# Performance work log

Measured on AMD Instinct MI355X. Metric: run time of the kernel, lower is better.

Reference implementation:

```python
import jax, jax.numpy as jnp
import numpy as np

N_CAT = 100000
N_USERS = 50000
D = 64
N_REL = 16  # edge_type in [1, 15]; weight has n_relations-1 = 15 rows
E = 1500000
NNZ = 1500000


def setup_inputs() -> dict:
    key = jax.random.key(0)
    k = jax.random.split(key, 8)
    category_emb = jax.random.normal(k[0], (N_CAT, D), dtype=jnp.float32)
    user_emb = jax.random.normal(k[1], (N_USERS, D), dtype=jnp.float32)
    edge_index = jax.random.randint(k[2], (2, E), 0, N_CAT, dtype=jnp.int32)
    edge_type = jax.random.randint(k[3], (E,), 1, N_REL, dtype=jnp.int32)  # [1, 15]
    iu = jax.random.randint(k[4], (NNZ,), 0, N_USERS, dtype=jnp.int32)
    ic = jax.random.randint(k[5], (NNZ,), 0, N_CAT, dtype=jnp.int32)
    interact_idx = jnp.stack([iu, ic], axis=0)
    interact_val = jax.random.uniform(k[6], (NNZ,), dtype=jnp.float32)
    weight = jax.random.normal(k[7], (N_REL - 1, D), dtype=jnp.float32) * (6.0 / (N_REL - 1 + D)) ** 0.5
    return {"category_emb": category_emb, "user_emb": user_emb,
            "edge_index": edge_index, "edge_type": edge_type,
            "interact_idx": interact_idx, "interact_val": interact_val,
            "weight": weight}


def reference(category_emb, user_emb, edge_index, edge_type, interact_idx, interact_val, weight):
    n_cat = category_emb.shape[0]
    n_users = user_emb.shape[0]
    head, tail = edge_index[0], edge_index[1]

    # per-edge relation embedding gather
    rel = weight[edge_type - 1]                       # [E, d]
    neigh = category_emb[tail] * rel                  # [E, d]

    # norm-based attention score per edge: (||h*r|| * ||t*r||)^2
    hn = jnp.linalg.norm(category_emb[head] * rel, axis=1)   # [E]
    tn = jnp.linalg.norm(neigh, axis=1)                      # [E]
    att = (hn * tn) ** 2                                     # [E]

    # scatter-softmax over head segments (score is constant across feature dim)
    seg_max = jax.ops.segment_max(att, head, num_segments=n_cat)
    e = jnp.exp(att - seg_max[head])
    seg_sum = jax.ops.segment_sum(e, head, num_segments=n_cat)
    w = e / seg_sum[head]                                    # [E]

    # scatter-sum aggregation of weighted neighbor messages
    category_agg = jax.ops.segment_sum(w[:, None] * neigh, head, num_segments=n_cat)  # [n_cat, d]

    # sparse-dense matmul: interact_mat @ category_emb (COO gather + segment_sum)
    iu, ic = interact_idx[0], interact_idx[1]
    user_agg = jax.ops.segment_sum(interact_val[:, None] * category_emb[ic], iu,
                                   num_segments=n_users)     # [n_users, d]

    # relation-score gating of user aggregation
    score = jax.nn.softmax(user_emb @ weight.T, axis=-1)     # [n_users, n_rel-1]
    user_agg = user_agg + (score @ weight) * user_agg
    return category_agg, user_agg
```

## Files before the change

kernel.cpp:

```cpp
#include <hip/hip_runtime.h>

#define N_CAT   100000
#define N_USERS 50000
#define DIM     64
#define N_RELM1 15
#define E_EDGES 1500000
#define NNZ_E   1500000

#define HPB   125
#define NB_H  800
#define UPB   80
#define NB_U  625
#define NB_T  (NB_H + NB_U)
#define CAP8  3072

#define NS_TILES 1563
#define GT_TILES 782

#define BIN_BLKS 256
#define BIN_CH   5860

#define NTL(p) __builtin_nontemporal_load(p)

__device__ __forceinline__ float sb2f(unsigned int v, int sh) {
    return (float)(int)(signed char)((v >> sh) & 0xFFu);
}

template <bool USE8>
__global__ void __launch_bounds__(256)
prep_kernel(const float* __restrict__ cat, const float* __restrict__ uemb,
            const float* __restrict__ weight,
            const int* __restrict__ head, const int* __restrict__ iu,
            float* __restrict__ normsq, unsigned int* __restrict__ cat8,
            float* __restrict__ scl,
            float* __restrict__ gfac, int* __restrict__ gcnt,
            int* __restrict__ cnts_cat, int* __restrict__ cnts_u0,
            int* __restrict__ cnts_u1) {
    __shared__ float smem[8320];
    int t = threadIdx.x;
    int lane = t & 63, wid = t >> 6;
    if (blockIdx.x < NS_TILES) {
        float* c2    = smem;
        float* w2t   = smem + 4160;
        float* nsqT  = smem + 5184;
        float* rinv  = smem + 6208;
        float* rmaxp = smem + 6272;
        int nbase = blockIdx.x * 64;
        int nclamp = min(64, N_CAT - nbase);
        for (int i = t; i < 1024; i += 256) {
            int d = i >> 4, r = i & 15;
            float w = (r < N_RELM1) ? weight[r * 64 + d] : 0.f;
            w2t[i] = w * w;
        }
        for (int i = t; i < 4096; i += 256) {
            int row = i >> 6, d = i & 63;
            float v = (row < nclamp) ? cat[(size_t)(nbase + row) * 64 + d] : 0.f;
            c2[row * 65 + d] = v;
        }
        __syncthreads();
        if (USE8) {
            {
                int row = t >> 2, part = t & 3;
                float m = 0.f;
#pragma unroll
                for (int d = part * 16; d < part * 16 + 16; ++d)
                    m = fmaxf(m, fabsf(c2[row * 65 + d]));
                rmaxp[t] = m;
            }
            __syncthreads();
            if (t < 64) {
                float m = fmaxf(fmaxf(rmaxp[4 * t], rmaxp[4 * t + 1]),
                                fmaxf(rmaxp[4 * t + 2], rmaxp[4 * t + 3]));
                rinv[t] = (m > 0.f) ? 127.f / m : 0.f;
                if (t < nclamp) scl[nbase + t] = (m > 0.f) ? m / 127.f : 0.f;
            }
            __syncthreads();
            for (int i = t; i < 1024; i += 256) {
                int row = i >> 4, q4 = i & 15;
                if (row < nclamp) {
                    float inv = rinv[row];
                    int d0 = q4 * 4;
                    unsigned int p = 0;
#pragma unroll
                    for (int k = 0; k < 4; ++k) {
                        int q = (int)rintf(c2[row * 65 + d0 + k] * inv);
                        p |= ((unsigned int)(q & 0xFF)) << (8 * k);
                    }
                    cat8[(size_t)(nbase + row) * 16 + q4] = p;
                }
            }
        }
        float a0 = 0, a1 = 0, a2 = 0, a3 = 0;
        int r0 = wid * 4;
#pragma unroll 8
        for (int d = 0; d < 64; ++d) {
            float c = c2[lane * 65 + d];
            float cc = c * c;
            float4 w4 = *(float4*)&w2t[d * 16 + r0];
            a0 += cc * w4.x; a1 += cc * w4.y; a2 += cc * w4.z; a3 += cc * w4.w;
        }
        nsqT[(r0 + 0) * 64 + lane] = a0;
        nsqT[(r0 + 1) * 64 + lane] = a1;
        nsqT[(r0 + 2) * 64 + lane] = a2;
        nsqT[(r0 + 3) * 64 + lane] = a3;
        __syncthreads();
        for (int i = t; i < nclamp * 15; i += 256) {
            int n = i / 15, r = i - n * 15;
            normsq[(size_t)(nbase + n) * 15 + r] = nsqT[r * 64 + n];
        }
    } else if (blockIdx.x < NS_TILES + GT_TILES) {
        float* ut  = smem;
        float* wt  = smem + 4160;
        float* wrT = smem + 5184;
        float* st  = smem + 6208;
        float* pt  = smem + 7232;
        int ub_ = (blockIdx.x - NS_TILES) * 64;
        int uclamp = min(64, N_USERS - ub_);
        for (int i = t; i < 1024; i += 256) {
            int d = i >> 4, r = i & 15;
            float w = (r < N_RELM1) ? weight[r * 64 + d] : 0.f;
            wt[i] = w;
            wrT[r * 64 + d] = w;
        }
        for (int i = t; i < 4096; i += 256) {
            int row = i >> 6, d = i & 63;
            ut[row * 65 + d] = (row < uclamp) ? uemb[(size_t)(ub_ + row) * 64 + d] : 0.f;
        }
        __syncthreads();
        float a0 = 0, a1 = 0, a2 = 0, a3 = 0;
        int r0 = wid * 4;
#pragma unroll 8
        for (int d = 0; d < 64; ++d) {
            float c = ut[lane * 65 + d];
            float4 w4 = *(float4*)&wt[d * 16 + r0];
            a0 += c * w4.x; a1 += c * w4.y; a2 += c * w4.z; a3 += c * w4.w;
        }
        st[lane * 16 + r0 + 0] = a0;
        st[lane * 16 + r0 + 1] = a1;
        st[lane * 16 + r0 + 2] = a2;
        st[lane * 16 + r0 + 3] = a3;
        __syncthreads();
        if (wid == 0) {
            float mx = -1e30f;
            float pv[N_RELM1];
#pragma unroll
            for (int r = 0; r < N_RELM1; ++r) mx = fmaxf(mx, st[lane * 16 + r]);
            float Z = 0.f;
#pragma unroll
            for (int r = 0; r < N_RELM1; ++r) { pv[r] = __expf(st[lane * 16 + r] - mx); Z += pv[r]; }
            float inv = 1.f / Z;
#pragma unroll
            for (int r = 0; r < N_RELM1; ++r) pt[lane * 16 + r] = pv[r] * inv;
        }
        __syncthreads();
        for (int i = t; i < uclamp * 64; i += 256) {
            int u = i >> 6, d = i & 63;
            float g = 0.f;
#pragma unroll
            for (int r = 0; r < N_RELM1; ++r) g += pt[u * 16 + r] * wrT[r * 64 + d];
            gfac[(size_t)(ub_ + u) * 64 + d] = g;
        }
    } else {
        int* ccnt = (int*)smem;
        int* cu0  = ccnt + NB_H;
        int* cu1  = cu0 + 640;
        for (int i = t; i < NB_H + 1280; i += 256) ccnt[i] = 0;
        __syncthreads();
        int hb = blockIdx.x - NS_TILES - GT_TILES;
        int c0 = hb * BIN_CH;
        int c1 = min(c0 + BIN_CH, E_EDGES);
        int hmid = c0 + BIN_CH / 2;
        for (int e = c0 + t; e < c1; e += 256) {
            atomicAdd(&ccnt[NTL(&head[e]) / HPB], 1);
            int ub = NTL(&iu[e]) / UPB;
            atomicAdd((e < hmid) ? &cu0[ub] : &cu1[ub], 1);
        }
        __syncthreads();
        for (int i = t; i < NB_H; i += 256) {
            int v = ccnt[i];
            cnts_cat[hb * NB_H + i] = v;
            if (v) atomicAdd(&gcnt[i], v);
        }
        for (int j = t; j < NB_U; j += 256) {
            int v0 = cu0[j], v1 = cu1[j];
            cnts_u0[hb * 640 + j] = v0;
            cnts_u1[hb * 640 + j] = v1;
            if (v0 + v1) atomicAdd(&gcnt[NB_H + j], v0 + v1);
        }
    }
}

__global__ void __launch_bounds__(1024)
bscan_kernel(const int* __restrict__ gcnt,
             int* __restrict__ hbase, int* __restrict__ ubase,
             int* __restrict__ cur) {
    __shared__ int wtot[16];
    int t = threadIdx.x, lane = t & 63, wv = t >> 6;
    int i0 = 2 * t, i1 = 2 * t + 1;
    int c0 = (i0 < NB_T) ? gcnt[i0] : 0;
    int c1 = (i1 < NB_T) ? gcnt[i1] : 0;
    int s = c0 + c1;
    int incl = s;
#pragma unroll
    for (int d = 1; d < 64; d <<= 1) {
        int v = __shfl_up(incl, d, 64);
        if (lane >= d) incl += v;
    }
    if (lane == 63) wtot[wv] = incl;
    __syncthreads();
    int woff = 0;
#pragma unroll
    for (int w = 0; w < 16; ++w) {
        int x = wtot[w];
        if (w < wv) woff += x;
    }
    int excl = woff + incl - s;
    if (i0 < NB_T) {
        if (i0 < NB_H) { hbase[i0] = excl; cur[i0] = excl; }
        else { int v = excl - E_EDGES; ubase[i0 - NB_H] = v; cur[i0] = v; }
    }
    int e1 = excl + c0;
    if (i1 < NB_T) {
        if (i1 < NB_H) { hbase[i1] = e1; cur[i1] = e1; }
        else { int v = e1 - E_EDGES; ubase[i1 - NB_H] = v; cur[i1] = v; }
    }
    if (t == 0) { hbase[NB_H] = E_EDGES; ubase[NB_U] = NNZ_E; }
}

__device__ __forceinline__ void block_scan_excl(const int* __restrict__ cnt,
                                                int* __restrict__ lofs, int n,
                                                int* __restrict__ wtot) {
    __syncthreads();
    int t = threadIdx.x, lane = t & 63, wv = t >> 6;
    int i0 = 2 * t, i1 = i0 + 1;
    int a0 = (i0 < n) ? cnt[i0] : 0;
    int a1 = (i1 < n) ? cnt[i1] : 0;
    int s = a0 + a1, incl = s;
#pragma unroll
    for (int d = 1; d < 64; d <<= 1) {
        int v = __shfl_up(incl, d, 64);
        if (lane >= d) incl += v;
    }
    if (lane == 63) wtot[wv] = incl;
    __syncthreads();
    int woff = 0;
#pragma unroll
    for (int w = 0; w < 16; ++w) { int x = wtot[w]; if (w < wv) woff += x; }
    int excl = woff + incl - s;
    if (i0 < n) lofs[i0] = excl;
    if (i1 < n) lofs[i1] = excl + a0;
    __syncthreads();
}

__global__ void __launch_bounds__(1024)
binning_kernel(const int* __restrict__ head, const int* __restrict__ tail,
               const int* __restrict__ etype,
               const int* __restrict__ iu, const int* __restrict__ ic,
               const float* __restrict__ ival,
               const int* __restrict__ cnts_cat, const int* __restrict__ cnts_u0,
               const int* __restrict__ cnts_u1,
               int* __restrict__ cur,
               int* __restrict__ ebinned, unsigned long long* __restrict__ nbinned) {
    __shared__ int scnt[NB_H];
    __shared__ int lofs[NB_H];
    __shared__ int gbase[NB_H];
    __shared__ int wtot[16];
    __shared__ int stage[BIN_CH];
    __shared__ unsigned short sbk[BIN_CH];
    int t = threadIdx.x;
    int hb = blockIdx.x;
    int c0 = hb * BIN_CH;
    int c1 = min(c0 + BIN_CH, E_EDGES);

    for (int i = t; i < NB_H; i += 1024) scnt[i] = NTL(&cnts_cat[hb * NB_H + i]);
    block_scan_excl(scnt, lofs, NB_H, wtot);
    for (int i = t; i < NB_H; i += 1024) {
        int c = scnt[i];
        gbase[i] = c ? atomicAdd(&cur[i], c) : 0;
    }
    __syncthreads();
    for (int i = t; i < NB_H; i += 1024) scnt[i] = 0;
    __syncthreads();
    for (int e = c0 + t; e < c1; e += 1024) {
        int h = NTL(&head[e]);
        int b = h / HPB;
        int r = atomicAdd(&scnt[b], 1);
        int slot = lofs[b] + r;
        stage[slot] = ((h - b * HPB) << 21) | (NTL(&tail[e]) << 4) | (NTL(&etype[e]) - 1);
        sbk[slot] = (unsigned short)b;
    }
    __syncthreads();
    int cn = c1 - c0;
    for (int s = t; s < cn; s += 1024) {
        int bk = sbk[s];
        ebinned[gbase[bk] + (s - lofs[bk])] = stage[s];
    }

    int2* stage2 = (int2*)stage;
    int2* nb2 = (int2*)nbinned;
#pragma unroll 1
    for (int half = 0; half < 2; ++half) {
        int h0 = c0 + half * (BIN_CH / 2);
        int h1 = min(h0 + BIN_CH / 2, E_EDGES);
        const int* crow = half ? cnts_u1 : cnts_u0;
        __syncthreads();
        for (int i = t; i < NB_U; i += 1024) scnt[i] = NTL(&crow[hb * 640 + i]);
        block_scan_excl(scnt, lofs, NB_U, wtot);
        for (int i = t; i < NB_U; i += 1024) {
            int c = scnt[i];
            gbase[i] = c ? atomicAdd(&cur[NB_H + i], c) : 0;
        }
        __syncthreads();
        for (int i = t; i < NB_U; i += 1024) scnt[i] = 0;
        __syncthreads();
        for (int e = h0 + t; e < h1; e += 1024) {
            int u = NTL(&iu[e]);
            int b = u / UPB;
            int r = atomicAdd(&scnt[b], 1);
            int slot = lofs[b] + r;
            stage2[slot] = make_int2(((u - b * UPB) << 17) | NTL(&ic[e]),
                                     __float_as_int(NTL(&ival[e])));
            sbk[slot] = (unsigned short)b;
        }
        __syncthreads();
        int hn = h1 - h0;
        for (int s = t; s < hn; s += 1024) {
            int bk = sbk[s];
            nb2[gbase[bk] + (s - lofs[bk])] = stage2[s];
        }
    }
}

template <bool USE8>
__global__ void __launch_bounds__(512)
fused_agg(const int* __restrict__ ebinned, const int* __restrict__ hbase,
          const unsigned long long* __restrict__ nbinned, const int* __restrict__ ubase,
          const float* __restrict__ normsq, const float* __restrict__ catf,
          const unsigned int* __restrict__ cat8, const float* __restrict__ scl,
          const float* __restrict__ weight,
          float* __restrict__ catagg, float* __restrict__ useragg) {
    __shared__ unsigned long long buf8[CAP8];
    __shared__ float4 wlds4[N_RELM1 * 16];
    __shared__ float hn[HPB * N_RELM1];
    __shared__ int cnt[HPB];
    __shared__ int ofs[HPB + 1];
    __shared__ unsigned int mxu[HPB];
    __shared__ float Zs[HPB];
    const float4* cfr = (const float4*)catf;
    int t = threadIdx.x;
    int wid = t >> 6, lane = t & 63;
    int qlane = lane & 15, qid = lane >> 4;

    if (blockIdx.x < NB_H) {
        int b = blockIdx.x;
        int s0 = hbase[b];
        int n = min(hbase[b + 1] - s0, CAP8);
        for (int i = t; i < N_RELM1 * 16; i += 512)
            wlds4[i] = ((const float4*)weight)[i];
        for (int i = t; i < HPB * N_RELM1; i += 512)
            hn[i] = normsq[(size_t)b * HPB * N_RELM1 + i];
        for (int i = t; i < HPB; i += 512) { cnt[i] = 0; mxu[i] = 0u; Zs[i] = 0.f; }
        __syncthreads();
        for (int i = t; i < n; i += 512)
            atomicAdd(&cnt[ebinned[s0 + i] >> 21], 1);
        __syncthreads();
        if (wid == 0) {
            int i0 = 2 * lane, i1 = 2 * lane + 1;
            int c0 = (i0 < HPB) ? cnt[i0] : 0;
            int c1 = (i1 < HPB) ? cnt[i1] : 0;
            int s = c0 + c1, incl = s;
#pragma unroll
            for (int d = 1; d < 64; d <<= 1) {
                int v = __shfl_up(incl, d, 64);
                if (lane >= d) incl += v;
            }
            int excl = incl - s;
            if (i0 <= HPB) ofs[i0] = excl;
            if (i1 <= HPB) ofs[i1] = excl + c0;
        }
        __syncthreads();
        for (int i = t; i < HPB; i += 512) cnt[i] = 0;
        __syncthreads();
        for (int i = t; i < n; i += 512) {
            int pk = ebinned[s0 + i];
            int hl = pk >> 21, tj = (pk >> 4) & 0x1FFFF, rj = pk & 15;
            float att = hn[hl * N_RELM1 + rj] * normsq[(size_t)tj * N_RELM1 + rj];
            int r = atomicAdd(&cnt[hl], 1);
            buf8[ofs[hl] + r] = ((unsigned long long)__float_as_uint(att) << 32) | (unsigned int)pk;
            atomicMax(&mxu[hl], __float_as_uint(att));
        }
        __syncthreads();
        for (int i = t; i < n; i += 512) {
            unsigned long long pay = buf8[i];
            int hl = ((int)(unsigned int)pay) >> 21;
            float att = __uint_as_float((unsigned int)(pay >> 32));
            float w = __expf(att - __uint_as_float(mxu[hl]));
            ((unsigned int*)buf8)[2 * i + 1] = __float_as_uint(w);
            atomicAdd(&Zs[hl], w);
        }
        __syncthreads();
        for (int hl = wid; hl < HPB; hl += 8) {
            int h = b * HPB + hl;
            int e0 = ofs[hl], e1 = ofs[hl + 1];
            float invZ = (e1 > e0) ? 1.f / Zs[hl] : 0.f;
            float ax = 0.f, ay = 0.f, az = 0.f, aw = 0.f;
            for (int j = e0; j < e1; j += 16) {
#pragma unroll
                for (int k = 0; k < 4; ++k) {
                    int idx = j + k * 4 + qid;
                    bool ok = idx < e1;
                    idx = ok ? idx : e0;
                    unsigned long long pay = buf8[idx];
                    int pk = (int)(unsigned int)pay;
                    float w = ok ? __uint_as_float((unsigned int)(pay >> 32)) : 0.f;
                    int tj = (pk >> 4) & 0x1FFFF, rj = pk & 15;
                    float4 wl = wlds4[rj * 16 + qlane];
                    if (USE8) {
                        unsigned int uv = cat8[(size_t)tj * 16 + qlane];
                        float ws = w * scl[tj];
                        ax += ws * sb2f(uv, 0)  * wl.x;
                        ay += ws * sb2f(uv, 8)  * wl.y;
                        az += ws * sb2f(uv, 16) * wl.z;
                        aw += ws * sb2f(uv, 24) * wl.w;
                    } else {
                        float4 cv = cfr[(size_t)tj * 16 + qlane];
                        ax += w * cv.x * wl.x;
                        ay += w * cv.y * wl.y;
                        az += w * cv.z * wl.z;
                        aw += w * cv.w * wl.w;
                    }
                }
            }
            ax += __shfl_xor(ax, 16, 64); ax += __shfl_xor(ax, 32, 64);
            ay += __shfl_xor(ay, 16, 64); ay += __shfl_xor(ay, 32, 64);
            az += __shfl_xor(az, 16, 64); az += __shfl_xor(az, 32, 64);
            aw += __shfl_xor(aw, 16, 64); aw += __shfl_xor(aw, 32, 64);
            if (lane < 16)
                ((float4*)catagg)[(size_t)h * 16 + qlane] =
                    make_float4(ax * invZ, ay * invZ, az * invZ, aw * invZ);
        }
    } else {
        int ub = blockIdx.x - NB_H;
        int s0 = ubase[ub];
        int n = min(ubase[ub + 1] - s0, CAP8);
        for (int i = t; i < UPB; i += 512) cnt[i] = 0;
        __syncthreads();
        for (int i = t; i < n; i += 512)
            atomicAdd(&cnt[((unsigned int)nbinned[s0 + i]) >> 17], 1);
        __syncthreads();
        if (wid == 0) {
            int i0 = 2 * lane, i1 = 2 * lane + 1;
            int c0 = (i0 < UPB) ? cnt[i0] : 0;
            int c1 = (i1 < UPB) ? cnt[i1] : 0;
            int s = c0 + c1, incl = s;
#pragma unroll
            for (int d = 1; d < 64; d <<= 1) {
                int v = __shfl_up(incl, d, 64);
                if (lane >= d) incl += v;
            }
            int excl = incl - s;
            if (i0 <= UPB) ofs[i0] = excl;
            if (i1 <= UPB) ofs[i1] = excl + c0;
        }
        __syncthreads();
        for (int i = t; i < UPB; i += 512) cnt[i] = 0;
        __syncthreads();
        for (int i = t; i < n; i += 512) {
            unsigned long long pay = nbinned[s0 + i];
            int ul = ((unsigned int)pay) >> 17;
            int r = atomicAdd(&cnt[ul], 1);
            buf8[ofs[ul] + r] = pay;
        }
        __syncthreads();
        for (int ul = wid; ul < UPB; ul += 8) {
            int u = ub * UPB + ul;
            int e0 = ofs[ul], e1 = ofs[ul + 1];
            float ax = 0.f, ay = 0.f, az = 0.f, aw = 0.f;
            for (int j = e0; j < e1; j += 32) {
#pragma unroll
                for (int k = 0; k < 8; ++k) {
                    int idx = j + k * 4 + qid;
                    bool ok = idx < e1;
                    idx = ok ? idx : e0;
                    unsigned long long pay = buf8[idx];
                    float v = ok ? __uint_as_float((unsigned int)(pay >> 32)) : 0.f;
                    int c = (int)((unsigned int)pay & 0x1FFFFu);
                    if (USE8) {
                        unsigned int uv = cat8[(size_t)c * 16 + qlane];
                        float vs = v * scl[c];
                        ax += vs * sb2f(uv, 0);
                        ay += vs * sb2f(uv, 8);
                        az += vs * sb2f(uv, 16);
                        aw += vs * sb2f(uv, 24);
                    } else {
                        float4 cv = cfr[(size_t)c * 16 + qlane];
                        ax += v * cv.x;
                        ay += v * cv.y;
                        az += v * cv.z;
                        aw += v * cv.w;
                    }
                }
            }
            ax += __shfl_xor(ax, 16, 64); ax += __shfl_xor(ax, 32, 64);
            ay += __shfl_xor(ay, 16, 64); ay += __shfl_xor(ay, 32, 64);
            az += __shfl_xor(az, 16, 64); az += __shfl_xor(az, 32, 64);
            aw += __shfl_xor(aw, 16, 64); aw += __shfl_xor(aw, 32, 64);
            if (lane < 16) {
                float4 gf = ((float4*)useragg)[(size_t)u * 16 + qlane];
                ((float4*)useragg)[(size_t)u * 16 + qlane] =
                    make_float4(ax * (1.f + gf.x), ay * (1.f + gf.y),
                                az * (1.f + gf.z), aw * (1.f + gf.w));
            }
        }
    }
}

extern "C" void kernel_launch(void* const* d_in, const int* in_sizes, int n_in,
                              void* d_out, int out_size, void* d_ws, size_t ws_size,
                              hipStream_t stream) {
    const float* cat    = (const float*)d_in[0];
    const float* uemb   = (const float*)d_in[1];
    const int*   eidx   = (const int*)d_in[2];
    const int*   etype  = (const int*)d_in[3];
    const int*   iidx   = (const int*)d_in[4];
    const float* ival   = (const float*)d_in[5];
    const float* weight = (const float*)d_in[6];

    float* catagg  = (float*)d_out;
    float* useragg = (float*)d_out + (size_t)N_CAT * DIM;

    int* ws = (int*)d_ws;
    float* normsq   = (float*)ws;
    int*   ebinned  = ws + 1500000;
    unsigned long long* nbinned = (unsigned long long*)(ws + 3000000);
    int*   gcnt     = ws + 6000000;
    int*   hbase    = ws + 6001425;
    int*   ubase    = ws + 6002226;
    int*   cur      = ws + 6002852;
    unsigned int* cat8 = (unsigned int*)(ws + 6004278);
    float* scl      = (float*)(ws + 6004278 + 1600000);
    const size_t NEED8 = (size_t)(6004278 + 1600000 + 100000) * 4;
    bool use8 = ws_size >= NEED8;

    int* dscr     = (int*)d_out;
    int* cnts_cat = dscr;
    int* cnts_u0  = dscr + 256 * NB_H;
    int* cnts_u1  = cnts_u0 + 256 * 640;

    const int* head = eidx;
    const int* tail = eidx + E_EDGES;
    const int* iu   = iidx;
    const int* ic   = iidx + NNZ_E;

    hipMemsetAsync(gcnt, 0, (size_t)NB_T * sizeof(int), stream);

    if (use8) {
        prep_kernel<true><<<NS_TILES + GT_TILES + BIN_BLKS, 256, 0, stream>>>(
            cat, uemb, weight, head, iu, normsq, cat8, scl, useragg, gcnt,
            cnts_cat, cnts_u0, cnts_u1);
    } else {
        prep_kernel<false><<<NS_TILES + GT_TILES + BIN_BLKS, 256, 0, stream>>>(
            cat, uemb, weight, head, iu, normsq, cat8, scl, useragg, gcnt,
            cnts_cat, cnts_u0, cnts_u1);
    }
    bscan_kernel<<<1, 1024, 0, stream>>>(gcnt, hbase, ubase, cur);
    binning_kernel<<<BIN_BLKS, 1024, 0, stream>>>(head, tail, etype, iu, ic, ival,
                                                  cnts_cat, cnts_u0, cnts_u1,
                                                  cur, ebinned, nbinned);
    if (use8) {
        fused_agg<true><<<NB_T, 512, 0, stream>>>(
            ebinned, hbase, nbinned, ubase, normsq, cat, cat8, scl, weight, catagg, useragg);
    } else {
        fused_agg<false><<<NB_T, 512, 0, stream>>>(
            ebinned, hbase, nbinned, ubase, normsq, cat, cat8, scl, weight, catagg, useragg);
    }
}
```

Measured before the change: 184.3 us.

## Widen int8 gathers to 8 bytes per lane and prefold row scales into weights

Gathers of the int8-quantized category rows now use uint2 loads, so each lane covers eight features and one wavefront processes eight edges at once instead of four. The per-row dequant scale is folded ahead of time, into the interaction value during binning and into the softmax weight before aggregation, which removes a dependent scl gather from the inner loops. The prep kernel also loads embedding tiles as float4. The cost is more accumulator registers and one extra shuffle-reduction level.

New measurement: 192.3 us. +4.3%, slower.

```diff
diff --git a/kernel.cpp b/kernel.cpp
--- a/kernel.cpp
+++ b/kernel.cpp
@@ -47,15 +47,20 @@
         float* rmaxp = smem + 6272;
         int nbase = blockIdx.x * 64;
         int nclamp = min(64, N_CAT - nbase);
+        const float4* cat4 = (const float4*)cat;
         for (int i = t; i < 1024; i += 256) {
             int d = i >> 4, r = i & 15;
             float w = (r < N_RELM1) ? weight[r * 64 + d] : 0.f;
             w2t[i] = w * w;
         }
-        for (int i = t; i < 4096; i += 256) {
-            int row = i >> 6, d = i & 63;
-            float v = (row < nclamp) ? cat[(size_t)(nbase + row) * 64 + d] : 0.f;
-            c2[row * 65 + d] = v;
+        for (int i = t; i < 1024; i += 256) {
+            int row = i >> 4, q = i & 15;
+            float4 v4 = (row < nclamp) ? cat4[(size_t)(nbase + row) * 16 + q]
+                                       : make_float4(0.f, 0.f, 0.f, 0.f);
+            c2[row * 65 + q * 4 + 0] = v4.x;
+            c2[row * 65 + q * 4 + 1] = v4.y;
+            c2[row * 65 + q * 4 + 2] = v4.z;
+            c2[row * 65 + q * 4 + 3] = v4.w;
         }
         __syncthreads();
         if (USE8) {
@@ -116,15 +121,21 @@
         float* pt  = smem + 7232;
         int ub_ = (blockIdx.x - NS_TILES) * 64;
         int uclamp = min(64, N_USERS - ub_);
+        const float4* ue4 = (const float4*)uemb;
         for (int i = t; i < 1024; i += 256) {
             int d = i >> 4, r = i & 15;
             float w = (r < N_RELM1) ? weight[r * 64 + d] : 0.f;
             wt[i] = w;
             wrT[r * 64 + d] = w;
         }
-        for (int i = t; i < 4096; i += 256) {
-            int row = i >> 6, d = i & 63;
-            ut[row * 65 + d] = (row < uclamp) ? uemb[(size_t)(ub_ + row) * 64 + d] : 0.f;
+        for (int i = t; i < 1024; i += 256) {
+            int row = i >> 4, q = i & 15;
+            float4 v4 = (row < uclamp) ? ue4[(size_t)(ub_ + row) * 16 + q]
+                                       : make_float4(0.f, 0.f, 0.f, 0.f);
+            ut[row * 65 + q * 4 + 0] = v4.x;
+            ut[row * 65 + q * 4 + 1] = v4.y;
+            ut[row * 65 + q * 4 + 2] = v4.z;
+            ut[row * 65 + q * 4 + 3] = v4.w;
         }
         __syncthreads();
         float a0 = 0, a1 = 0, a2 = 0, a3 = 0;
@@ -252,11 +263,12 @@
     __syncthreads();
 }
 
+template <bool USE8>
 __global__ void __launch_bounds__(1024)
 binning_kernel(const int* __restrict__ head, const int* __restrict__ tail,
                const int* __restrict__ etype,
                const int* __restrict__ iu, const int* __restrict__ ic,
-               const float* __restrict__ ival,
+               const float* __restrict__ ival, const float* __restrict__ scl,
                const int* __restrict__ cnts_cat, const int* __restrict__ cnts_u0,
                const int* __restrict__ cnts_u1,
                int* __restrict__ cur,
@@ -318,8 +330,10 @@
             int b = u / UPB;
             int r = atomicAdd(&scnt[b], 1);
             int slot = lofs[b] + r;
-            stage2[slot] = make_int2(((u - b * UPB) << 17) | NTL(&ic[e]),
-                                     __float_as_int(NTL(&ival[e])));
+            int cix = NTL(&ic[e]);
+            float v = NTL(&ival[e]);
+            if (USE8) v *= scl[cix];
+            stage2[slot] = make_int2(((u - b * UPB) << 17) | cix, __float_as_int(v));
             sbk[slot] = (unsigned short)b;
         }
         __syncthreads();
@@ -347,9 +361,11 @@
     __shared__ unsigned int mxu[HPB];
     __shared__ float Zs[HPB];
     const float4* cfr = (const float4*)catf;
+    const uint2* c8r2 = (const uint2*)cat8;
     int t = threadIdx.x;
     int wid = t >> 6, lane = t & 63;
     int qlane = lane & 15, qid = lane >> 4;
+    int olane = lane & 7, oid = lane >> 3;
 
     if (blockIdx.x < NB_H) {
         int b = blockIdx.x;
@@ -392,10 +408,12 @@
         __syncthreads();
         for (int i = t; i < n; i += 512) {
             unsigned long long pay = buf8[i];
-            int hl = ((int)(unsigned int)pay) >> 21;
+            int pk = (int)(unsigned int)pay;
+            int hl = pk >> 21;
             float att = __uint_as_float((unsigned int)(pay >> 32));
             float w = __expf(att - __uint_as_float(mxu[hl]));
-            ((unsigned int*)buf8)[2 * i + 1] = __float_as_uint(w);
+            float wstore = USE8 ? w * scl[(pk >> 4) & 0x1FFFF] : w;
+            ((unsigned int*)buf8)[2 * i + 1] = __float_as_uint(wstore);
             atomicAdd(&Zs[hl], w);
         }
         __syncthreads();
@@ -403,41 +421,72 @@
             int h = b * HPB + hl;
             int e0 = ofs[hl], e1 = ofs[hl + 1];
             float invZ = (e1 > e0) ? 1.f / Zs[hl] : 0.f;
-            float ax = 0.f, ay = 0.f, az = 0.f, aw = 0.f;
-            for (int j = e0; j < e1; j += 16) {
-#pragma unroll
-                for (int k = 0; k < 4; ++k) {
-                    int idx = j + k * 4 + qid;
-                    bool ok = idx < e1;
-                    idx = ok ? idx : e0;
-                    unsigned long long pay = buf8[idx];
-                    int pk = (int)(unsigned int)pay;
-                    float w = ok ? __uint_as_float((unsigned int)(pay >> 32)) : 0.f;
-                    int tj = (pk >> 4) & 0x1FFFF, rj = pk & 15;
-                    float4 wl = wlds4[rj * 16 + qlane];
-                    if (USE8) {
-                        unsigned int uv = cat8[(size_t)tj * 16 + qlane];
-                        float ws = w * scl[tj];
-                        ax += ws * sb2f(uv, 0)  * wl.x;
-                        ay += ws * sb2f(uv, 8)  * wl.y;
-                        az += ws * sb2f(uv, 16) * wl.z;
-                        aw += ws * sb2f(uv, 24) * wl.w;
-                    } else {
+            if (USE8) {
+                float a0 = 0, a1 = 0, a2 = 0, a3 = 0, a4 = 0, a5 = 0, a6 = 0, a7 = 0;
+                for (int j = e0; j < e1; j += 16) {
+#pragma unroll
+                    for (int k = 0; k < 2; ++k) {
+                        int idx = j + k * 8 + oid;
+                        bool ok = idx < e1;
+                        idx = ok ? idx : e0;
+                        unsigned long long pay = buf8[idx];
+                        int pk = (int)(unsigned int)pay;
+                        float ws = ok ? __uint_as_float((unsigned int)(pay >> 32)) : 0.f;
+                        int tj = (pk >> 4) & 0x1FFFF, rj = pk & 15;
+                        uint2 uv = c8r2[(size_t)tj * 8 + olane];
+                        float4 wl0 = wlds4[rj * 16 + olane * 2];
+                        float4 wl1 = wlds4[rj * 16 + olane * 2 + 1];
+                        a0 += ws * sb2f(uv.x, 0)  * wl0.x;
+                        a1 += ws * sb2f(uv.x, 8)  * wl0.y;
+                        a2 += ws * sb2f(uv.x, 16) * wl0.z;
+                        a3 += ws * sb2f(uv.x, 24) * wl0.w;
+                        a4 += ws * sb2f(uv.y, 0)  * wl1.x;
+                        a5 += ws * sb2f(uv.y, 8)  * wl1.y;
+                        a6 += ws * sb2f(uv.y, 16) * wl1.z;
+                        a7 += ws * sb2f(uv.y, 24) * wl1.w;
+                    }
+                }
+#pragma unroll
+                for (int d = 8; d <= 32; d <<= 1) {
+                    a0 += __shfl_xor(a0, d, 64); a1 += __shfl_xor(a1, d, 64);
+                    a2 += __shfl_xor(a2, d, 64); a3 += __shfl_xor(a3, d, 64);
+                    a4 += __shfl_xor(a4, d, 64); a5 += __shfl_xor(a5, d, 64);
+                    a6 += __shfl_xor(a6, d, 64); a7 += __shfl_xor(a7, d, 64);
+                }
+                if (oid == 0) {
+                    ((float4*)catagg)[(size_t)h * 16 + olane * 2] =
+                        make_float4(a0 * invZ, a1 * invZ, a2 * invZ, a3 * invZ);
+                    ((float4*)catagg)[(size_t)h * 16 + olane * 2 + 1] =
+                        make_float4(a4 * invZ, a5 * invZ, a6 * invZ, a7 * invZ);
+                }
+            } else {
+                float ax = 0.f, ay = 0.f, az = 0.f, aw = 0.f;
+                for (int j = e0; j < e1; j += 16) {
+#pragma unroll
+                    for (int k = 0; k < 4; ++k) {
+                        int idx = j + k * 4 + qid;
+                        bool ok = idx < e1;
+                        idx = ok ? idx : e0;
+                        unsigned long long pay = buf8[idx];
+                        int pk = (int)(unsigned int)pay;
+                        float w = ok ? __uint_as_float((unsigned int)(pay >> 32)) : 0.f;
+                        int tj = (pk >> 4) & 0x1FFFF, rj = pk & 15;
                         float4 cv = cfr[(size_t)tj * 16 + qlane];
+                        float4 wl = wlds4[rj * 16 + qlane];
                         ax += w * cv.x * wl.x;
                         ay += w * cv.y * wl.y;
                         az += w * cv.z * wl.z;
                         aw += w * cv.w * wl.w;
                     }
                 }
+                ax += __shfl_xor(ax, 16, 64); ax += __shfl_xor(ax, 32, 64);
+                ay += __shfl_xor(ay, 16, 64); ay += __shfl_xor(ay, 32, 64);
+                az += __shfl_xor(az, 16, 64); az += __shfl_xor(az, 32, 64);
+                aw += __shfl_xor(aw, 16, 64); aw += __shfl_xor(aw, 32, 64);
+                if (lane < 16)
+                    ((float4*)catagg)[(size_t)h * 16 + qlane] =
+                        make_float4(ax * invZ, ay * invZ, az * invZ, aw * invZ);
             }
-            ax += __shfl_xor(ax, 16, 64); ax += __shfl_xor(ax, 32, 64);
-            ay += __shfl_xor(ay, 16, 64); ay += __shfl_xor(ay, 32, 64);
-            az += __shfl_xor(az, 16, 64); az += __shfl_xor(az, 32, 64);
-            aw += __shfl_xor(aw, 16, 64); aw += __shfl_xor(aw, 32, 64);
-            if (lane < 16)
-                ((float4*)catagg)[(size_t)h * 16 + qlane] =
-                    make_float4(ax * invZ, ay * invZ, az * invZ, aw * invZ);
         }
     } else {
         int ub = blockIdx.x - NB_H;
@@ -475,24 +524,56 @@
         for (int ul = wid; ul < UPB; ul += 8) {
             int u = ub * UPB + ul;
             int e0 = ofs[ul], e1 = ofs[ul + 1];
-            float ax = 0.f, ay = 0.f, az = 0.f, aw = 0.f;
-            for (int j = e0; j < e1; j += 32) {
-#pragma unroll
-                for (int k = 0; k < 8; ++k) {
-                    int idx = j + k * 4 + qid;
-                    bool ok = idx < e1;
-                    idx = ok ? idx : e0;
-                    unsigned long long pay = buf8[idx];
-                    float v = ok ? __uint_as_float((unsigned int)(pay >> 32)) : 0.f;
-                    int c = (int)((unsigned int)pay & 0x1FFFFu);
-                    if (USE8) {
-                        unsigned int uv = cat8[(size_t)c * 16 + qlane];
-                        float vs = v * scl[c];
-                        ax += vs * sb2f(uv, 0);
-                        ay += vs * sb2f(uv, 8);
-                        az += vs * sb2f(uv, 16);
-                        aw += vs * sb2f(uv, 24);
-                    } else {
+            if (USE8) {
+                float a0 = 0, a1 = 0, a2 = 0, a3 = 0, a4 = 0, a5 = 0, a6 = 0, a7 = 0;
+                for (int j = e0; j < e1; j += 32) {
+#pragma unroll
+                    for (int k = 0; k < 4; ++k) {
+                        int idx = j + k * 8 + oid;
+                        bool ok = idx < e1;
+                        idx = ok ? idx : e0;
+                        unsigned long long pay = buf8[idx];
+                        float vs = ok ? __uint_as_float((unsigned int)(pay >> 32)) : 0.f;
+                        int c = (int)((unsigned int)pay & 0x1FFFFu);
+                        uint2 uv = c8r2[(size_t)c * 8 + olane];
+                        a0 += vs * sb2f(uv.x, 0);
+                        a1 += vs * sb2f(uv.x, 8);
+                        a2 += vs * sb2f(uv.x, 16);
+                        a3 += vs * sb2f(uv.x, 24);
+                        a4 += vs * sb2f(uv.y, 0);
+                        a5 += vs * sb2f(uv.y, 8);
+                        a6 += vs * sb2f(uv.y, 16);
+                        a7 += vs * sb2f(uv.y, 24);
+                    }
+                }
+#pragma unroll
+                for (int d = 8; d <= 32; d <<= 1) {
+                    a0 += __shfl_xor(a0, d, 64); a1 += __shfl_xor(a1, d, 64);
+                    a2 += __shfl_xor(a2, d, 64); a3 += __shfl_xor(a3, d, 64);
+                    a4 += __shfl_xor(a4, d, 64); a5 += __shfl_xor(a5, d, 64);
+                    a6 += __shfl_xor(a6, d, 64); a7 += __shfl_xor(a7, d, 64);
+                }
+                if (oid == 0) {
+                    float4 g0 = ((float4*)useragg)[(size_t)u * 16 + olane * 2];
+                    float4 g1 = ((float4*)useragg)[(size_t)u * 16 + olane * 2 + 1];
+                    ((float4*)useragg)[(size_t)u * 16 + olane * 2] =
+                        make_float4(a0 * (1.f + g0.x), a1 * (1.f + g0.y),
+                                    a2 * (1.f + g0.z), a3 * (1.f + g0.w));
+                    ((float4*)useragg)[(size_t)u * 16 + olane * 2 + 1] =
+                        make_float4(a4 * (1.f + g1.x), a5 * (1.f + g1.y),
+                                    a6 * (1.f + g1.z), a7 * (1.f + g1.w));
+                }
+            } else {
+                float ax = 0.f, ay = 0.f, az = 0.f, aw = 0.f;
+                for (int j = e0; j < e1; j += 32) {
+#pragma unroll
+                    for (int k = 0; k < 8; ++k) {
+                        int idx = j + k * 4 + qid;
+                        bool ok = idx < e1;
+                        idx = ok ? idx : e0;
+                        unsigned long long pay = buf8[idx];
+                        float v = ok ? __uint_as_float((unsigned int)(pay >> 32)) : 0.f;
+                        int c = (int)((unsigned int)pay & 0x1FFFFu);
                         float4 cv = cfr[(size_t)c * 16 + qlane];
                         ax += v * cv.x;
                         ay += v * cv.y;
@@ -500,16 +581,16 @@
                         aw += v * cv.w;
                     }
                 }
-            }
-            ax += __shfl_xor(ax, 16, 64); ax += __shfl_xor(ax, 32, 64);
-            ay += __shfl_xor(ay, 16, 64); ay += __shfl_xor(ay, 32, 64);
-            az += __shfl_xor(az, 16, 64); az += __shfl_xor(az, 32, 64);
-            aw += __shfl_xor(aw, 16, 64); aw += __shfl_xor(aw, 32, 64);
-            if (lane < 16) {
-                float4 gf = ((float4*)useragg)[(size_t)u * 16 + qlane];
-                ((float4*)useragg)[(size_t)u * 16 + qlane] =
-                    make_float4(ax * (1.f + gf.x), ay * (1.f + gf.y),
-                                az * (1.f + gf.z), aw * (1.f + gf.w));
+                ax += __shfl_xor(ax, 16, 64); ax += __shfl_xor(ax, 32, 64);
+                ay += __shfl_xor(ay, 16, 64); ay += __shfl_xor(ay, 32, 64);
+                az += __shfl_xor(az, 16, 64); az += __shfl_xor(az, 32, 64);
+                aw += __shfl_xor(aw, 16, 64); aw += __shfl_xor(aw, 32, 64);
+                if (lane < 16) {
+                    float4 gf = ((float4*)useragg)[(size_t)u * 16 + qlane];
+                    ((float4*)useragg)[(size_t)u * 16 + qlane] =
+                        make_float4(ax * (1.f + gf.x), ay * (1.f + gf.y),
+                                    az * (1.f + gf.z), aw * (1.f + gf.w));
+                }
             }
         }
     }
@@ -558,19 +639,20 @@
         prep_kernel<true><<<NS_TILES + GT_TILES + BIN_BLKS, 256, 0, stream>>>(
             cat, uemb, weight, head, iu, normsq, cat8, scl, useragg, gcnt,
             cnts_cat, cnts_u0, cnts_u1);
+        bscan_kernel<<<1, 1024, 0, stream>>>(gcnt, hbase, ubase, cur);
+        binning_kernel<true><<<BIN_BLKS, 1024, 0, stream>>>(
+            head, tail, etype, iu, ic, ival, scl,
+            cnts_cat, cnts_u0, cnts_u1, cur, ebinned, nbinned);
+        fused_agg<true><<<NB_T, 512, 0, stream>>>(
+            ebinned, hbase, nbinned, ubase, normsq, cat, cat8, scl, weight, catagg, useragg);
     } else {
         prep_kernel<false><<<NS_TILES + GT_TILES + BIN_BLKS, 256, 0, stream>>>(
             cat, uemb, weight, head, iu, normsq, cat8, scl, useragg, gcnt,
             cnts_cat, cnts_u0, cnts_u1);
-    }
-    bscan_kernel<<<1, 1024, 0, stream>>>(gcnt, hbase, ubase, cur);
-    binning_kernel<<<BIN_BLKS, 1024, 0, stream>>>(head, tail, etype, iu, ic, ival,
-                                                  cnts_cat, cnts_u0, cnts_u1,
-                                                  cur, ebinned, nbinned);
-    if (use8) {
-        fused_agg<true><<<NB_T, 512, 0, stream>>>(
-            ebinned, hbase, nbinned, ubase, normsq, cat, cat8, scl, weight, catagg, useragg);
-    } else {
+        bscan_kernel<<<1, 1024, 0, stream>>>(gcnt, hbase, ubase, cur);
+        binning_kernel<false><<<BIN_BLKS, 1024, 0, stream>>>(
+            head, tail, etype, iu, ic, ival, scl,
+            cnts_cat, cnts_u0, cnts_u1, cur, ebinned, nbinned);
         fused_agg<false><<<NB_T, 512, 0, stream>>>(
             ebinned, hbase, nbinned, ubase, normsq, cat, cat8, scl, weight, catagg, useragg);
     }
```
